# Kernel tuning notes

Hardware: AMD Instinct MI355X
Metric: run time of the kernel (lower is better)

## Reference

```python
import jax, jax.numpy as jnp
import numpy as np

B, N, M = 16, 512, 512
VS, QS, OS, H = 2048, 1024, 2048, 16
DH = OS // H  # per-head dim


def setup_inputs() -> dict:
    key = jax.random.key(0)
    ks = jax.random.split(key, 8)
    s = lambda fan_in: 1.0 / np.sqrt(fan_in)
    return {
        "v": jax.random.normal(ks[0], (B, N, VS), jnp.float32),
        "q": jax.random.normal(ks[1], (B, M, QS), jnp.float32),
        "v_mask": jnp.ones((B, N), jnp.float32),
        "q_mask": jnp.ones((B, M), jnp.float32),
        "Wv": jax.random.normal(ks[2], (VS, 3 * OS), jnp.float32) * s(VS),
        "bv": jnp.zeros((3 * OS,), jnp.float32),
        "Wq": jax.random.normal(ks[3], (QS, 3 * OS), jnp.float32) * s(QS),
        "bq": jnp.zeros((3 * OS,), jnp.float32),
        "Wvo": jax.random.normal(ks[4], (OS + VS, OS), jnp.float32) * s(OS + VS),
        "bvo": jnp.zeros((OS,), jnp.float32),
        "Wqo": jax.random.normal(ks[5], (OS + QS, OS), jnp.float32) * s(OS + QS),
        "bqo": jnp.zeros((OS,), jnp.float32),
    }


def _heads(x):
    # [B, L, OS] -> [B, L, H, DH]; torch.split over dim 2 == contiguous head slices
    return x.reshape(x.shape[0], x.shape[1], H, DH)


def reference(v, q, v_mask, q_mask, Wv, bv, Wq, bq, Wvo, bvo, Wqo, bqo):
    # FCNet = relu(Linear)
    v_trans = jax.nn.relu(v @ Wv + bv) * v_mask[:, :, None]
    q_trans = jax.nn.relu(q @ Wq + bq) * q_mask[:, :, None]
    v_key, v_qry, v_val = (_heads(t) for t in jnp.split(v_trans, 3, axis=2))
    q_key, q_qry, q_val = (_heads(t) for t in jnp.split(q_trans, 3, axis=2))
    scale = 1.0 / np.sqrt(DH)
    neg_inf = jnp.float32(-jnp.inf)

    # q2v: visual queries attend over question keys -> [B, H, N, M]
    q2v = jnp.einsum("bnhd,bmhd->bhnm", v_qry, q_key) * scale
    q2v = jnp.where(q_mask[:, None, None, :] == 0, neg_inf, q2v)
    v_update = jnp.einsum("bhnm,bmhd->bnhd", jax.nn.softmax(q2v, axis=-1), q_val)
    v_update = v_update.reshape(B, N, OS)

    # v2q: question queries attend over visual keys -> [B, H, M, N]
    v2q = jnp.einsum("bmhd,bnhd->bhmn", q_qry, v_key) * scale
    v2q = jnp.where(v_mask[:, None, None, :] == 0, neg_inf, v2q)
    q_update = jnp.einsum("bhmn,bnhd->bmhd", jax.nn.softmax(v2q, axis=-1), v_val)
    q_update = q_update.reshape(B, M, OS)

    updated_v = jax.nn.relu(jnp.concatenate([v, v_update], axis=2) @ Wvo + bvo)
    updated_q = jax.nn.relu(jnp.concatenate([q, q_update], axis=2) @ Wqo + bqo)
    return updated_v, updated_q
```

## Files before the change

kernel.cpp:

```cpp
#include <hip/hip_runtime.h>
#include <hip/hip_bf16.h>
#include <cstdint>


typedef __hip_bfloat16 bf16;
typedef __attribute__((ext_vector_type(8))) __bf16 bf16x8;
typedef __attribute__((ext_vector_type(4))) float f32x4;
typedef __attribute__((ext_vector_type(4))) unsigned short us4;
typedef __attribute__((ext_vector_type(8))) unsigned short us8;

#define AS1 __attribute__((address_space(1)))
#define AS3 __attribute__((address_space(3)))

__device__ __forceinline__ void gl_lds16(const bf16* g, bf16* l) {
    __builtin_amdgcn_global_load_lds((AS1 void*)(uintptr_t)(g), (AS3 void*)(l), 16, 0, 0);
}

__device__ __forceinline__ bf16x8 ld8(const bf16* p) { return *(const bf16x8*)p; }

__device__ __forceinline__ f32x4 mfma16(bf16x8 a, bf16x8 b, f32x4 c) {
    return __builtin_amdgcn_mfma_f32_16x16x32_bf16(a, b, c, 0, 0, 0);
}

__device__ __forceinline__ unsigned short f2bs(float f) {
    unsigned u = __builtin_bit_cast(unsigned, f);
    unsigned r = u + 0x7FFFu + ((u >> 16) & 1u);
    return (unsigned short)(r >> 16);
}

__global__ __launch_bounds__(256) void cvt_cols_k(
    const float* __restrict__ src, bf16* __restrict__ dst,
    int cprShift, int dstStride, int totalChunks)
{
    const int id = blockIdx.x * 256 + threadIdx.x;
    if (id >= totalChunks) return;
    const int row = id >> cprShift;
    const int cc = (id - (row << cprShift)) << 3;
    const float* s = src + ((size_t)row << (cprShift + 3)) + cc;
    const float4 a = *(const float4*)s;
    const float4 b = *(const float4*)(s + 4);
    us8 o;
    o[0] = f2bs(a.x); o[1] = f2bs(a.y); o[2] = f2bs(a.z); o[3] = f2bs(a.w);
    o[4] = f2bs(b.x); o[5] = f2bs(b.y); o[6] = f2bs(b.z); o[7] = f2bs(b.w);
    *(us8*)(dst + (size_t)row * dstStride + cc) = o;
}

__global__ __launch_bounds__(256) void cvt_transpose_k(
    const float* __restrict__ in, unsigned short* __restrict__ out,
    int inStride, int outStride)
{
    __shared__ unsigned short tile[64][65];
    const int ti = blockIdx.x * 64;
    const int tj = blockIdx.y * 64;
    const int t = threadIdx.x;
    const int r = t >> 4;
    const int c4 = (t & 15) << 2;
#pragma unroll
    for (int i = 0; i < 4; ++i) {
        const float4 v = *(const float4*)(in + (size_t)(tj + r + i * 16) * inStride + ti + c4);
        tile[r + i * 16][c4 + 0] = f2bs(v.x);
        tile[r + i * 16][c4 + 1] = f2bs(v.y);
        tile[r + i * 16][c4 + 2] = f2bs(v.z);
        tile[r + i * 16][c4 + 3] = f2bs(v.w);
    }
    __syncthreads();
#pragma unroll
    for (int i = 0; i < 4; ++i) {
        const int orow = ti + r + i * 16;
        us4 v;
        v[0] = tile[c4 + 0][r + i * 16];
        v[1] = tile[c4 + 1][r + i * 16];
        v[2] = tile[c4 + 2][r + i * 16];
        v[3] = tile[c4 + 3][r + i * 16];
        *(us4*)(out + (size_t)orow * outStride + tj + c4) = v;
    }
}

__global__ __launch_bounds__(256) void transpose_k(
    const unsigned short* __restrict__ in, unsigned short* __restrict__ out,
    int inStride, int outStride, size_t inOffB, int inOffH, size_t outSliceStride)
{
    __shared__ unsigned short tile[64][65];
    const int z = blockIdx.z;
    const unsigned short* inp = in + (size_t)(z >> 4) * inOffB + (size_t)(z & 15) * inOffH;
    unsigned short* outp = out + (size_t)z * outSliceStride;
    const int ti = blockIdx.x * 64;
    const int tj = blockIdx.y * 64;
    const int t = threadIdx.x;
    const int r = t >> 4;
    const int c4 = (t & 15) << 2;
#pragma unroll
    for (int i = 0; i < 4; ++i) {
        us4 v = *(const us4*)(inp + (size_t)(tj + r + i * 16) * inStride + ti + c4);
        tile[r + i * 16][c4 + 0] = v[0];
        tile[r + i * 16][c4 + 1] = v[1];
        tile[r + i * 16][c4 + 2] = v[2];
        tile[r + i * 16][c4 + 3] = v[3];
    }
    __syncthreads();
#pragma unroll
    for (int i = 0; i < 4; ++i) {
        const int orow = ti + r + i * 16;
        us4 v;
        v[0] = tile[c4 + 0][r + i * 16];
        v[1] = tile[c4 + 1][r + i * 16];
        v[2] = tile[c4 + 2][r + i * 16];
        v[3] = tile[c4 + 3][r + i * 16];
        *(us4*)(outp + (size_t)orow * outStride + tj + c4) = v;
    }
}

template <typename OutT>
__global__ __launch_bounds__(256) void gemm_bt(
    const bf16* __restrict__ A, const bf16* __restrict__ BT,
    const float* __restrict__ bias, const float* __restrict__ mask,
    OutT* __restrict__ C, int K, int lda, int ldb, int ldc)
{
    __shared__ __align__(16) bf16 smem[8192];
    bf16* As = smem;
    bf16* Bs = smem + 4096;
    const int tid = threadIdx.x;
    const int lane = tid & 63;
    const int l16 = lane & 15;
    const int quad = lane >> 4;
    const int wave = tid >> 6;
    const int wr = (wave >> 1) * 64;
    const int wc = (wave & 1) * 64;
    const size_t row0 = (size_t)blockIdx.y * 128;
    const size_t col0 = (size_t)blockIdx.x * 128;

    const f32x4 z4 = {0.f, 0.f, 0.f, 0.f};
    f32x4 acc[4][4];
#pragma unroll
    for (int r = 0; r < 4; ++r)
#pragma unroll
        for (int c = 0; c < 4; ++c) acc[r][c] = z4;

    const int e1 = tid * 8;
    const int m1 = e1 >> 5, k1 = e1 & 31;
    const int e2 = e1 + 2048;
    const int m2 = e2 >> 5, k2 = e2 & 31;

    for (int k0 = 0; k0 < K; k0 += 32) {
        gl_lds16(A  + (row0 + m1) * lda + k0 + k1, As + e1);
        gl_lds16(A  + (row0 + m2) * lda + k0 + k2, As + e2);
        gl_lds16(BT + (col0 + m1) * ldb + k0 + k1, Bs + e1);
        gl_lds16(BT + (col0 + m2) * ldb + k0 + k2, Bs + e2);
        __syncthreads();
        bf16x8 af[4], bfv[4];
#pragma unroll
        for (int r = 0; r < 4; ++r)
            af[r] = ld8(As + (wr + r * 16 + l16) * 32 + quad * 8);
#pragma unroll
        for (int c = 0; c < 4; ++c)
            bfv[c] = ld8(Bs + (wc + c * 16 + l16) * 32 + quad * 8);
#pragma unroll
        for (int r = 0; r < 4; ++r)
#pragma unroll
            for (int c = 0; c < 4; ++c)
                acc[r][c] = mfma16(af[r], bfv[c], acc[r][c]);
        __syncthreads();
    }

    float bcol[4];
#pragma unroll
    for (int c = 0; c < 4; ++c) bcol[c] = bias[col0 + wc + c * 16 + l16];

    if constexpr (sizeof(OutT) == 2) {
        bf16* stg = smem;
#pragma unroll
        for (int p = 0; p < 4; ++p) {
            if (wr == (p >> 1) * 64) {
#pragma unroll
                for (int rr = 0; rr < 2; ++rr) {
                    const int r = (p & 1) * 2 + rr;
#pragma unroll
                    for (int c = 0; c < 4; ++c) {
                        const int lcol = wc + c * 16 + l16;
#pragma unroll
                        for (int g = 0; g < 4; ++g) {
                            const int lrow = rr * 16 + quad * 4 + g;
                            const size_t grow = row0 + wr + r * 16 + quad * 4 + g;
                            float v = acc[r][c][g] + bcol[c];
                            v = v > 0.f ? v : 0.f;
                            if (mask) v *= mask[grow];
                            ((unsigned short*)stg)[lrow * 136 + lcol] = f2bs(v);
                        }
                    }
                }
            }
            asm volatile("" ::: "memory");
            __syncthreads();
            const int srow = tid >> 3;
            const int scol = (tid & 7) * 16;
            const us8 o0 = *(const us8*)((unsigned short*)stg + srow * 136 + scol);
            const us8 o1 = *(const us8*)((unsigned short*)stg + srow * 136 + scol + 8);
            OutT* dst = C + (row0 + p * 32 + srow) * ldc + col0 + scol;
            *(us8*)dst = o0;
            *(us8*)(dst + 8) = o1;
            __syncthreads();
        }
    } else {
        float* stg = (float*)smem;
#pragma unroll
        for (int p = 0; p < 8; ++p) {
            if (wr == (p >> 2) * 64) {
                const int r = p & 3;
#pragma unroll
                for (int c = 0; c < 4; ++c) {
                    const int lcol = wc + c * 16 + l16;
#pragma unroll
                    for (int g = 0; g < 4; ++g) {
                        const int lrow = quad * 4 + g;
                        const size_t grow = row0 + wr + r * 16 + quad * 4 + g;
                        float v = acc[r][c][g] + bcol[c];
                        v = v > 0.f ? v : 0.f;
                        if (mask) v *= mask[grow];
                        stg[lrow * 132 + lcol] = v;
                    }
                }
            }
            asm volatile("" ::: "memory");
            __syncthreads();
            const int srow = tid >> 4;
            const int scol = (tid & 15) * 8;
            const f32x4 o0 = *(const f32x4*)(stg + srow * 132 + scol);
            const f32x4 o1 = *(const f32x4*)(stg + srow * 132 + scol + 4);
            OutT* dst = C + (row0 + p * 16 + srow) * ldc + col0 + scol;
            *(f32x4*)dst = o0;
            *(f32x4*)(dst + 4) = o1;
            __syncthreads();
        }
    }
}

__global__ __launch_bounds__(128) void attn_k(
    const bf16* __restrict__ Q, const bf16* __restrict__ Kk,
    const bf16* __restrict__ VT, const float* __restrict__ kmask,
    bf16* __restrict__ Out,
    int Lq, int Lk, int qStride, int kStride, int outStride, int outColOff)
{
    const int bh = blockIdx.y;
    const int b = bh >> 4, h = bh & 15;
    const int n0 = blockIdx.x * 32;
    const int tid = threadIdx.x;
    const int wave = tid >> 6, lane = tid & 63;
    const int l16 = lane & 15, quad = lane >> 4;

    __shared__ __align__(16) bf16 smem[16640 + 8192];
    bf16* kv = smem + 16640;

#pragma unroll
    for (int i = 0; i < 4; ++i) {
        const int e = i * 1024 + tid * 8;
        const int r = e >> 7, d = e & 127;
        gl_lds16(Q + (size_t)(b * Lq + n0 + r) * qStride + h * 128 + d, smem + e);
    }
    __syncthreads();

    bf16x8 aq[4];
#pragma unroll
    for (int ks = 0; ks < 4; ++ks)
        aq[ks] = ld8(smem + (wave * 16 + l16) * 128 + ks * 32 + quad * 8);
    __syncthreads();

    const bf16* Kb = Kk + (size_t)b * Lk * kStride + h * 128;
    f32x4 S[32];
    const int swz = (l16 & 7);
#pragma unroll
    for (int kt = 0; kt < 8; ++kt) {
#pragma unroll
        for (int c = 0; c < 8; ++c) {
            const int e = c * 1024 + tid * 8;
            const int r = e >> 7;
            const int j = (e >> 3) & 15;
            gl_lds16(Kb + (size_t)(kt * 64 + r) * kStride + ((j ^ (r & 7)) << 3), kv + e);
        }
        __syncthreads();
        __builtin_amdgcn_s_setprio(1);
#pragma unroll
        for (int tt = 0; tt < 4; ++tt) {
            const int row = tt * 16 + l16;
            f32x4 c2 = {0.f, 0.f, 0.f, 0.f};
#pragma unroll
            for (int ks = 0; ks < 4; ++ks)
                c2 = mfma16(aq[ks], ld8(kv + row * 128 + (((ks * 4 + quad) ^ swz) << 3)), c2);
            S[kt * 4 + tt] = c2;
        }
        __builtin_amdgcn_s_setprio(0);
        __syncthreads();
    }

    const float scale = 0.08838834764831845f;
    float mx[4] = {-3.0e38f, -3.0e38f, -3.0e38f, -3.0e38f};
#pragma unroll
    for (int t = 0; t < 32; ++t)
#pragma unroll
        for (int g = 0; g < 4; ++g) mx[g] = fmaxf(mx[g], S[t][g]);
#pragma unroll
    for (int off = 1; off < 16; off <<= 1)
#pragma unroll
        for (int g = 0; g < 4; ++g) mx[g] = fmaxf(mx[g], __shfl_xor(mx[g], off));

    float sm[4] = {0.f, 0.f, 0.f, 0.f};
    const float* mrow = kmask + (size_t)b * Lk;
#pragma unroll
    for (int t = 0; t < 32; ++t) {
        const float mv = mrow[t * 16 + l16];
#pragma unroll
        for (int g = 0; g < 4; ++g) {
            float p = (mv != 0.f) ? __expf((S[t][g] - mx[g]) * scale) : 0.f;
            S[t][g] = p;
            sm[g] += p;
        }
    }
#pragma unroll
    for (int off = 1; off < 16; off <<= 1)
#pragma unroll
        for (int g = 0; g < 4; ++g) sm[g] += __shfl_xor(sm[g], off);
    float rs[4];
#pragma unroll
    for (int g = 0; g < 4; ++g) rs[g] = 1.f / sm[g];

    bf16* pw = smem + wave * 8320;
#pragma unroll
    for (int t = 0; t < 32; ++t) {
        const int col = t * 16 + l16;
#pragma unroll
        for (int g = 0; g < 4; ++g)
            pw[(quad * 4 + g) * 520 + col] = __float2bfloat16(S[t][g] * rs[g]);
    }
    asm volatile("" ::: "memory");
    __syncthreads();

    bf16x8 pa[16];
#pragma unroll
    for (int ks = 0; ks < 16; ++ks)
        pa[ks] = ld8(pw + l16 * 520 + ks * 32 + quad * 8);

    const bf16* Vb = VT + (size_t)bh * 128 * Lk;
    const size_t orow = (size_t)b * Lq + n0 + wave * 16 + quad * 4;
    for (int dt = 0; dt < 8; ++dt) {
#pragma unroll
        for (int c = 0; c < 8; ++c) {
            const int e = c * 1024 + tid * 8;
            const int r = e >> 9;
            const int j = (e >> 3) & 63;
            gl_lds16(Vb + (size_t)(dt * 16 + r) * Lk + ((j ^ (r & 7)) << 3), kv + e);
        }
        __syncthreads();
        __builtin_amdgcn_s_setprio(1);
        f32x4 c2 = {0.f, 0.f, 0.f, 0.f};
#pragma unroll
        for (int ks = 0; ks < 16; ++ks)
            c2 = mfma16(pa[ks], ld8(kv + l16 * 512 + (((ks * 4 + quad) ^ swz) << 3)), c2);
        __builtin_amdgcn_s_setprio(0);
        const int col = outColOff + h * 128 + dt * 16 + l16;
#pragma unroll
        for (int g = 0; g < 4; ++g)
            Out[(orow + g) * outStride + col] = __float2bfloat16(c2[g]);
        __syncthreads();
    }
}

extern "C" void kernel_launch(void* const* d_in, const int* in_sizes, int n_in,
                              void* d_out, int out_size, void* d_ws, size_t ws_size,
                              hipStream_t stream)
{
    (void)in_sizes; (void)n_in; (void)out_size; (void)ws_size;
    const float* v   = (const float*)d_in[0];
    const float* q   = (const float*)d_in[1];
    const float* vm  = (const float*)d_in[2];
    const float* qm  = (const float*)d_in[3];
    const float* Wv  = (const float*)d_in[4];
    const float* bv  = (const float*)d_in[5];
    const float* Wq  = (const float*)d_in[6];
    const float* bq  = (const float*)d_in[7];
    const float* Wvo = (const float*)d_in[8];
    const float* bvo = (const float*)d_in[9];
    const float* Wqo = (const float*)d_in[10];
    const float* bqo = (const float*)d_in[11];

    float* out_v = (float*)d_out;
    float* out_q = out_v + (size_t)8192 * 2048;

    bf16* ws = (bf16*)d_ws;
    bf16* v_trans = ws; ws += (size_t)8192 * 6144;
    bf16* q_trans = ws; ws += (size_t)8192 * 6144;
    bf16* vcat    = ws; ws += (size_t)8192 * 4096;
    bf16* qcat    = ws; ws += (size_t)8192 * 3072;
    bf16* WvT     = ws; ws += (size_t)6144 * 2048;
    bf16* WqT     = ws; ws += (size_t)6144 * 1024;
    bf16* WvoT    = ws; ws += (size_t)2048 * 4096;
    bf16* WqoT    = ws; ws += (size_t)2048 * 3072;
    bf16* VvalT   = ws; ws += (size_t)256 * 128 * 512;
    bf16* QvalT   = ws; ws += (size_t)256 * 128 * 512;

    cvt_cols_k<<<8192, 256, 0, stream>>>(v, vcat, 8, 4096, 8192 * 256);
    cvt_cols_k<<<4096, 256, 0, stream>>>(q, qcat, 7, 3072, 8192 * 128);

    cvt_transpose_k<<<dim3(96, 32), 256, 0, stream>>>(Wv,  (unsigned short*)WvT,  6144, 2048);
    cvt_transpose_k<<<dim3(96, 16), 256, 0, stream>>>(Wq,  (unsigned short*)WqT,  6144, 1024);
    cvt_transpose_k<<<dim3(32, 64), 256, 0, stream>>>(Wvo, (unsigned short*)WvoT, 2048, 4096);
    cvt_transpose_k<<<dim3(32, 48), 256, 0, stream>>>(Wqo, (unsigned short*)WqoT, 2048, 3072);

    gemm_bt<bf16><<<dim3(48, 64), 256, 0, stream>>>(vcat, WvT, bv, vm, v_trans, 2048, 4096, 2048, 6144);
    gemm_bt<bf16><<<dim3(48, 64), 256, 0, stream>>>(qcat, WqT, bq, qm, q_trans, 1024, 3072, 1024, 6144);

    transpose_k<<<dim3(2, 8, 256), 256, 0, stream>>>((const unsigned short*)(v_trans + 4096), (unsigned short*)VvalT,
                                                     6144, 512, (size_t)512 * 6144, 128, 65536);
    transpose_k<<<dim3(2, 8, 256), 256, 0, stream>>>((const unsigned short*)(q_trans + 4096), (unsigned short*)QvalT,
                                                     6144, 512, (size_t)512 * 6144, 128, 65536);

    attn_k<<<dim3(16, 256), 128, 0, stream>>>(v_trans + 2048, q_trans, QvalT, qm, vcat,
                                              512, 512, 6144, 6144, 4096, 2048);
    attn_k<<<dim3(16, 256), 128, 0, stream>>>(q_trans + 2048, v_trans, VvalT, vm, qcat,
                                              512, 512, 6144, 6144, 3072, 1024);

    gemm_bt<float><<<dim3(16, 64), 256, 0, stream>>>(vcat, WvoT, bvo, nullptr, out_v, 4096, 4096, 4096, 2048);
    gemm_bt<float><<<dim3(16, 64), 256, 0, stream>>>(qcat, WqoT, bqo, nullptr, out_q, 3072, 3072, 3072, 2048);
}
```

Baseline: 1.598 ms.

## Rewrite GEMM with 256x256 tiles, triple-buffered LDS prefetch and swizzled layout

The bf16 GEMM now uses 512-thread blocks computing 256x256 output tiles, with each wave owning 128x64. It triple-buffers K-slices in LDS, issuing global-to-LDS loads two steps ahead with fine-grained vmcnt waits instead of a full sync each step. It also XOR-swizzles the LDS layout to cut bank conflicts and raises MFMA priority with setprio. The aim is to hide memory latency, raise arithmetic intensity and reduce barrier stalls. The costs are more registers and LDS (96KB per block), which limit occupancy, and fewer blocks for the smaller output GEMMs.

Measured after the change: 1.365 ms. 14.5% less time.

```diff
diff --git a/kernel.cpp b/kernel.cpp
--- a/kernel.cpp
+++ b/kernel.cpp
@@ -111,90 +111,143 @@
 }
 
 template <typename OutT>
-__global__ __launch_bounds__(256) void gemm_bt(
+__global__ __launch_bounds__(512, 2) void gemm_bt(
     const bf16* __restrict__ A, const bf16* __restrict__ BT,
     const float* __restrict__ bias, const float* __restrict__ mask,
     OutT* __restrict__ C, int K, int lda, int ldb, int ldc)
 {
-    __shared__ __align__(16) bf16 smem[8192];
-    bf16* As = smem;
-    bf16* Bs = smem + 4096;
+    __shared__ __align__(16) bf16 smem[49152];
     const int tid = threadIdx.x;
     const int lane = tid & 63;
     const int l16 = lane & 15;
     const int quad = lane >> 4;
     const int wave = tid >> 6;
-    const int wr = (wave >> 1) * 64;
-    const int wc = (wave & 1) * 64;
-    const size_t row0 = (size_t)blockIdx.y * 128;
-    const size_t col0 = (size_t)blockIdx.x * 128;
+    const int wm = wave >> 2;
+    const int wn = wave & 3;
+    const int rofs = ((quad ^ ((l16 >> 1) & 3)) << 3);
+    const size_t row0 = (size_t)blockIdx.y * 256;
+    const size_t col0 = (size_t)blockIdx.x * 256;
+
+    const int ci0 = tid, ci1 = 512 + tid;
+    const int ra0 = ci0 >> 2, ja0 = ci0 & 3;
+    const int ra1 = ci1 >> 2, ja1 = ci1 & 3;
+    const bf16* Asrc0 = A + (row0 + ra0) * lda + ((ja0 ^ ((ra0 >> 1) & 3)) << 3);
+    const bf16* Asrc1 = A + (row0 + ra1) * lda + ((ja1 ^ ((ra1 >> 1) & 3)) << 3);
+    const bf16* Bsrc0 = BT + (col0 + ra0) * ldb + ((ja0 ^ ((ra0 >> 1) & 3)) << 3);
+    const bf16* Bsrc1 = BT + (col0 + ra1) * ldb + ((ja1 ^ ((ra1 >> 1) & 3)) << 3);
+
+    bf16* b0 = smem;
+    bf16* b1 = smem + 16384;
+    bf16* b2 = smem + 32768;
 
     const f32x4 z4 = {0.f, 0.f, 0.f, 0.f};
-    f32x4 acc[4][4];
-#pragma unroll
-    for (int r = 0; r < 4; ++r)
+    f32x4 acc[8][4];
+#pragma unroll
+    for (int r = 0; r < 8; ++r)
 #pragma unroll
         for (int c = 0; c < 4; ++c) acc[r][c] = z4;
 
-    const int e1 = tid * 8;
-    const int m1 = e1 >> 5, k1 = e1 & 31;
-    const int e2 = e1 + 2048;
-    const int m2 = e2 >> 5, k2 = e2 & 31;
-
-    for (int k0 = 0; k0 < K; k0 += 32) {
-        gl_lds16(A  + (row0 + m1) * lda + k0 + k1, As + e1);
-        gl_lds16(A  + (row0 + m2) * lda + k0 + k2, As + e2);
-        gl_lds16(BT + (col0 + m1) * ldb + k0 + k1, Bs + e1);
-        gl_lds16(BT + (col0 + m2) * ldb + k0 + k2, Bs + e2);
-        __syncthreads();
-        bf16x8 af[4], bfv[4];
-#pragma unroll
-        for (int r = 0; r < 4; ++r)
-            af[r] = ld8(As + (wr + r * 16 + l16) * 32 + quad * 8);
-#pragma unroll
-        for (int c = 0; c < 4; ++c)
-            bfv[c] = ld8(Bs + (wc + c * 16 + l16) * 32 + quad * 8);
-#pragma unroll
-        for (int r = 0; r < 4; ++r)
-#pragma unroll
-            for (int c = 0; c < 4; ++c)
-                acc[r][c] = mfma16(af[r], bfv[c], acc[r][c]);
-        __syncthreads();
-    }
+    const int nt = K >> 5;
+
+    gl_lds16(Asrc0, b0 + ci0 * 8);
+    gl_lds16(Asrc1, b0 + ci1 * 8);
+    gl_lds16(Bsrc0, b0 + 8192 + ci0 * 8);
+    gl_lds16(Bsrc1, b0 + 8192 + ci1 * 8);
+    gl_lds16(Asrc0 + 32, b1 + ci0 * 8);
+    gl_lds16(Asrc1 + 32, b1 + ci1 * 8);
+    gl_lds16(Bsrc0 + 32, b1 + 8192 + ci0 * 8);
+    gl_lds16(Bsrc1 + 32, b1 + 8192 + ci1 * 8);
+    asm volatile("s_waitcnt vmcnt(4)" ::: "memory");
+    __builtin_amdgcn_s_barrier();
+    asm volatile("" ::: "memory");
+
+    bf16* cur = b0; bf16* nxt = b1; bf16* nx2 = b2;
+    for (int t = 0; t < nt; ++t) {
+        const bool st = (t + 2) < nt;
+        const int kofs = (t + 2) << 5;
+        const bf16* aRd = cur + (wm * 128 + l16) * 32 + rofs;
+        const bf16* bRd = cur + 8192 + (wn * 64 + l16) * 32 + rofs;
+
+        if (st) {
+            gl_lds16(Asrc0 + kofs, nx2 + ci0 * 8);
+            gl_lds16(Asrc1 + kofs, nx2 + ci1 * 8);
+        }
+        bf16x8 bfr[4];
+#pragma unroll
+        for (int fc = 0; fc < 4; ++fc) bfr[fc] = ld8(bRd + fc * 512);
+        bf16x8 af[4];
+#pragma unroll
+        for (int fr = 0; fr < 4; ++fr) af[fr] = ld8(aRd + fr * 512);
+        __builtin_amdgcn_s_setprio(1);
+#pragma unroll
+        for (int fr = 0; fr < 4; ++fr)
+#pragma unroll
+            for (int fc = 0; fc < 4; ++fc)
+                acc[fr][fc] = mfma16(af[fr], bfr[fc], acc[fr][fc]);
+        __builtin_amdgcn_s_setprio(0);
+        asm volatile("" ::: "memory");
+        __builtin_amdgcn_s_barrier();
+        asm volatile("" ::: "memory");
+
+        if (st) {
+            gl_lds16(Bsrc0 + kofs, nx2 + 8192 + ci0 * 8);
+            gl_lds16(Bsrc1 + kofs, nx2 + 8192 + ci1 * 8);
+        }
+#pragma unroll
+        for (int fr = 0; fr < 4; ++fr) af[fr] = ld8(aRd + 2048 + fr * 512);
+        __builtin_amdgcn_s_setprio(1);
+#pragma unroll
+        for (int fr = 0; fr < 4; ++fr)
+#pragma unroll
+            for (int fc = 0; fc < 4; ++fc)
+                acc[fr + 4][fc] = mfma16(af[fr], bfr[fc], acc[fr + 4][fc]);
+        __builtin_amdgcn_s_setprio(0);
+
+        if (t + 1 < nt) {
+            if (st) asm volatile("s_waitcnt vmcnt(4)" ::: "memory");
+            else    asm volatile("s_waitcnt vmcnt(0)" ::: "memory");
+            __builtin_amdgcn_s_barrier();
+            asm volatile("" ::: "memory");
+        }
+        bf16* tmp = cur; cur = nxt; nxt = nx2; nx2 = tmp;
+    }
+
+    asm volatile("" ::: "memory");
+    __syncthreads();
 
     float bcol[4];
 #pragma unroll
-    for (int c = 0; c < 4; ++c) bcol[c] = bias[col0 + wc + c * 16 + l16];
+    for (int fc = 0; fc < 4; ++fc) bcol[fc] = bias[col0 + wn * 64 + fc * 16 + l16];
 
     if constexpr (sizeof(OutT) == 2) {
-        bf16* stg = smem;
-#pragma unroll
-        for (int p = 0; p < 4; ++p) {
-            if (wr == (p >> 1) * 64) {
-#pragma unroll
-                for (int rr = 0; rr < 2; ++rr) {
-                    const int r = (p & 1) * 2 + rr;
-#pragma unroll
-                    for (int c = 0; c < 4; ++c) {
-                        const int lcol = wc + c * 16 + l16;
+        unsigned short* stg = (unsigned short*)smem;
+#pragma unroll
+        for (int p = 0; p < 8; ++p) {
+            if (wm == (p >> 2)) {
+#pragma unroll
+                for (int d = 0; d < 2; ++d) {
+                    const int fr = (p & 3) * 2 + d;
+#pragma unroll
+                    for (int fc = 0; fc < 4; ++fc) {
+                        const int lcol = wn * 64 + fc * 16 + l16;
 #pragma unroll
                         for (int g = 0; g < 4; ++g) {
-                            const int lrow = rr * 16 + quad * 4 + g;
-                            const size_t grow = row0 + wr + r * 16 + quad * 4 + g;
-                            float v = acc[r][c][g] + bcol[c];
+                            const int lrow = d * 16 + quad * 4 + g;
+                            const size_t grow = row0 + (size_t)p * 32 + lrow;
+                            float v = acc[fr][fc][g] + bcol[fc];
                             v = v > 0.f ? v : 0.f;
                             if (mask) v *= mask[grow];
-                            ((unsigned short*)stg)[lrow * 136 + lcol] = f2bs(v);
+                            stg[lrow * 264 + lcol] = f2bs(v);
                         }
                     }
                 }
             }
             asm volatile("" ::: "memory");
             __syncthreads();
-            const int srow = tid >> 3;
-            const int scol = (tid & 7) * 16;
-            const us8 o0 = *(const us8*)((unsigned short*)stg + srow * 136 + scol);
-            const us8 o1 = *(const us8*)((unsigned short*)stg + srow * 136 + scol + 8);
+            const int srow = tid >> 4;
+            const int scol = (tid & 15) * 16;
+            const us8 o0 = *(const us8*)(stg + srow * 264 + scol);
+            const us8 o1 = *(const us8*)(stg + srow * 264 + scol + 8);
             OutT* dst = C + (row0 + p * 32 + srow) * ldc + col0 + scol;
             *(us8*)dst = o0;
             *(us8*)(dst + 8) = o1;
@@ -204,31 +257,35 @@
         float* stg = (float*)smem;
 #pragma unroll
         for (int p = 0; p < 8; ++p) {
-            if (wr == (p >> 2) * 64) {
-                const int r = p & 3;
-#pragma unroll
-                for (int c = 0; c < 4; ++c) {
-                    const int lcol = wc + c * 16 + l16;
-#pragma unroll
-                    for (int g = 0; g < 4; ++g) {
-                        const int lrow = quad * 4 + g;
-                        const size_t grow = row0 + wr + r * 16 + quad * 4 + g;
-                        float v = acc[r][c][g] + bcol[c];
-                        v = v > 0.f ? v : 0.f;
-                        if (mask) v *= mask[grow];
-                        stg[lrow * 132 + lcol] = v;
+            if (wm == (p >> 2)) {
+#pragma unroll
+                for (int d = 0; d < 2; ++d) {
+                    const int fr = (p & 3) * 2 + d;
+#pragma unroll
+                    for (int fc = 0; fc < 4; ++fc) {
+                        const int lcol = wn * 64 + fc * 16 + l16;
+#pragma unroll
+                        for (int g = 0; g < 4; ++g) {
+                            const int lrow = d * 16 + quad * 4 + g;
+                            const size_t grow = row0 + (size_t)p * 32 + lrow;
+                            float v = acc[fr][fc][g] + bcol[fc];
+                            v = v > 0.f ? v : 0.f;
+                            if (mask) v *= mask[grow];
+                            stg[lrow * 260 + lcol] = v;
+                        }
                     }
                 }
             }
             asm volatile("" ::: "memory");
             __syncthreads();
             const int srow = tid >> 4;
-            const int scol = (tid & 15) * 8;
-            const f32x4 o0 = *(const f32x4*)(stg + srow * 132 + scol);
-            const f32x4 o1 = *(const f32x4*)(stg + srow * 132 + scol + 4);
-            OutT* dst = C + (row0 + p * 16 + srow) * ldc + col0 + scol;
-            *(f32x4*)dst = o0;
-            *(f32x4*)(dst + 4) = o1;
+            const int scol = (tid & 15) * 16;
+            float* dst = (float*)C + (row0 + p * 32 + srow) * ldc + col0 + scol;
+            const float* s = stg + srow * 260 + scol;
+            *(f32x4*)(dst + 0)  = *(const f32x4*)(s + 0);
+            *(f32x4*)(dst + 4)  = *(const f32x4*)(s + 4);
+            *(f32x4*)(dst + 8)  = *(const f32x4*)(s + 8);
+            *(f32x4*)(dst + 12) = *(const f32x4*)(s + 12);
             __syncthreads();
         }
     }
@@ -404,8 +461,8 @@
     cvt_transpose_k<<<dim3(32, 64), 256, 0, stream>>>(Wvo, (unsigned short*)WvoT, 2048, 4096);
     cvt_transpose_k<<<dim3(32, 48), 256, 0, stream>>>(Wqo, (unsigned short*)WqoT, 2048, 3072);
 
-    gemm_bt<bf16><<<dim3(48, 64), 256, 0, stream>>>(vcat, WvT, bv, vm, v_trans, 2048, 4096, 2048, 6144);
-    gemm_bt<bf16><<<dim3(48, 64), 256, 0, stream>>>(qcat, WqT, bq, qm, q_trans, 1024, 3072, 1024, 6144);
+    gemm_bt<bf16><<<dim3(24, 32), 512, 0, stream>>>(vcat, WvT, bv, vm, v_trans, 2048, 4096, 2048, 6144);
+    gemm_bt<bf16><<<dim3(24, 32), 512, 0, stream>>>(qcat, WqT, bq, qm, q_trans, 1024, 3072, 1024, 6144);
 
     transpose_k<<<dim3(2, 8, 256), 256, 0, stream>>>((const unsigned short*)(v_trans + 4096), (unsigned short*)VvalT,
                                                      6144, 512, (size_t)512 * 6144, 128, 65536);
@@ -417,6 +474,6 @@
     attn_k<<<dim3(16, 256), 128, 0, stream>>>(q_trans + 2048, v_trans, VvalT, vm, qcat,
                                               512, 512, 6144, 6144, 3072, 1024);
 
-    gemm_bt<float><<<dim3(16, 64), 256, 0, stream>>>(vcat, WvoT, bvo, nullptr, out_v, 4096, 4096, 4096, 2048);
-    gemm_bt<float><<<dim3(16, 64), 256, 0, stream>>>(qcat, WqoT, bqo, nullptr, out_q, 3072, 3072, 3072, 2048);
-}
+    gemm_bt<float><<<dim3(8, 32), 512, 0, stream>>>(vcat, WvoT, bvo, nullptr, out_v, 4096, 4096, 4096, 2048);
+    gemm_bt<float><<<dim3(8, 32), 512, 0, stream>>>(qcat, WqoT, bqo, nullptr, out_q, 3072, 3072, 3072, 2048);
+}
```
